# Optimization experiments

Hardware: AMD Instinct MI355X
Metric: run time of the kernel (lower is better)

## Reference

```python
import jax, jax.numpy as jnp
import numpy as np

D_MODEL = 1024


def setup_inputs() -> dict:
    key = jax.random.key(0)
    kx, kq, kk, kv = jax.random.split(key, 4)
    x = jax.random.normal(kx, (4, 2048, D_MODEL), dtype=jnp.float32)
    s = 1.0 / np.sqrt(D_MODEL)
    # torch nn.Linear weight is [out, in]; y = x @ W.T
    Wq = jax.random.normal(kq, (D_MODEL, D_MODEL), dtype=jnp.float32) * s
    Wk = jax.random.normal(kk, (D_MODEL, D_MODEL), dtype=jnp.float32) * s
    Wv = jax.random.normal(kv, (D_MODEL, D_MODEL), dtype=jnp.float32) * s
    return {"x": x, "Wq": Wq, "Wk": Wk, "Wv": Wv}


def reference(x, Wq, Wk, Wv):
    # Linear projections (no bias): [b, s, d]
    Q = jnp.einsum("bsd,ed->bse", x, Wq)
    K = jnp.einsum("bsd,ed->bse", x, Wk)
    V = jnp.einsum("bsd,ed->bse", x, Wv)
    d_k = Q.shape[-1]
    scores = jnp.einsum("bqd,bkd->bqk", Q, K) / jnp.sqrt(jnp.asarray(d_k, Q.dtype))
    weights = jax.nn.softmax(scores, axis=-1)
    return jnp.einsum("bqk,bkd->bqd", weights, V)
```

## Files before the change

### kernel.cpp

```cpp
#include <hip/hip_runtime.h>
#include <hip/hip_bf16.h>

using bf16 = __hip_bfloat16;
typedef __attribute__((ext_vector_type(8))) short short8;
typedef __attribute__((ext_vector_type(16))) float f32x16;

__global__ __launch_bounds__(256) void cast_all(const float* __restrict__ x,
                                                const float* __restrict__ Wq,
                                                const float* __restrict__ Wk,
                                                const float* __restrict__ Wv,
                                                bf16* __restrict__ xb, bf16* __restrict__ Wb) {
  const int b = blockIdx.x;
  const float* src;
  bf16* dst;
  if (b < 8192) {
    src = x + (size_t)b * 1024;
    dst = xb + (size_t)b * 1024;
  } else if (b < 9216) {
    src = Wq + (size_t)(b - 8192) * 1024;
    dst = Wb + (size_t)(b - 8192) * 1024;
  } else if (b < 10240) {
    src = Wk + (size_t)(b - 9216) * 1024;
    dst = Wb + (size_t)(b - 8192) * 1024;
  } else {
    src = Wv + (size_t)(b - 10240) * 1024;
    dst = Wb + (size_t)(b - 8192) * 1024;
  }
  const int i = threadIdx.x * 4;
  const float4 f = *(const float4*)(src + i);
  bf16 h[4];
  h[0] = __float2bfloat16(f.x);
  h[1] = __float2bfloat16(f.y);
  h[2] = __float2bfloat16(f.z);
  h[3] = __float2bfloat16(f.w);
  *(uint2*)(dst + i) = *(const uint2*)h;
}

template <int BN, class Epi>
__device__ __forceinline__ void gemm_nt(const bf16* __restrict__ A, const bf16* __restrict__ B,
                                        int lda, int ldb, int K, int m0, int n0, Epi epi) {
  constexpr int THREADS = BN * 2;
  constexpr int NA = 8192 / (THREADS * 16);
  constexpr int NB = (BN * 64) / (THREADS * 16);
  constexpr int L = NA + NB;
  constexpr int SLOT = (128 + BN) * 64;
  __shared__ char smem[3 * SLOT];
  const int t = threadIdx.x;
  const int lane = t & 63;
  const int wave = t >> 6;
  const int wm = (BN == 256) ? (wave >> 2) * 64 : (wave >> 1) * 64;
  const int wn = (BN == 256) ? (wave & 3) * 64 : (wave & 1) * 64;
  const int rl = lane & 31;
  const int grp = lane >> 5;

  f32x16 acc[2][2];
#pragma unroll
  for (int i = 0; i < 2; ++i)
#pragma unroll
    for (int j = 0; j < 2; ++j)
#pragma unroll
      for (int r = 0; r < 16; ++r) acc[i][j][r] = 0.f;

  const bf16* gA[NA];
#pragma unroll
  for (int j = 0; j < NA; ++j) {
    const int s = j * THREADS + t;
    const int row = s >> 2;
    const int f = (row + (row >> 2)) & 3;
    gA[j] = A + (size_t)(m0 + row) * lda + ((((s & 3) ^ f)) << 3);
  }
  const bf16* gB[NB];
#pragma unroll
  for (int j = 0; j < NB; ++j) {
    const int s = j * THREADS + t;
    const int row = s >> 2;
    const int f = (row + (row >> 2)) & 3;
    gB[j] = B + (size_t)(n0 + row) * ldb + ((((s & 3) ^ f)) << 3);
  }

  auto stage = [&](int kt, int slot) {
    char* base = smem + slot * SLOT;
    bf16* As = (bf16*)base;
    bf16* Bs = (bf16*)(base + 8192);
    const int k0 = kt * 32;
#pragma unroll
    for (int j = 0; j < NA; ++j)
      __builtin_amdgcn_global_load_lds(
          (const __attribute__((address_space(1))) unsigned int*)(gA[j] + k0),
          (__attribute__((address_space(3))) unsigned int*)(As + (j * THREADS + wave * 64) * 8),
          16, 0, 0);
#pragma unroll
    for (int j = 0; j < NB; ++j)
      __builtin_amdgcn_global_load_lds(
          (const __attribute__((address_space(1))) unsigned int*)(gB[j] + k0),
          (__attribute__((address_space(3))) unsigned int*)(Bs + (j * THREADS + wave * 64) * 8),
          16, 0, 0);
  };

  const int NT = K >> 5;

  stage(0, 0);
  stage(1, 1);
  if constexpr (L == 3) {
    asm volatile("s_waitcnt vmcnt(3)" ::: "memory");
  } else {
    asm volatile("s_waitcnt vmcnt(4)" ::: "memory");
  }
  __builtin_amdgcn_s_barrier();
  __builtin_amdgcn_sched_barrier(0);

  int s0 = 0;
  for (int kt = 0; kt < NT; ++kt) {
    const int s1 = (s0 == 2) ? 0 : s0 + 1;
    const int s2 = (s1 == 2) ? 0 : s1 + 1;
    const char* base = smem + s0 * SLOT;
    const bf16* As = (const bf16*)base;
    const bf16* Bs = (const bf16*)(base + 8192);

    if (kt + 2 < NT) stage(kt + 2, s2);

    short8 af[2][2], bv[2][2];
#pragma unroll
    for (int ks = 0; ks < 2; ++ks) {
      const int kb = ks * 2 + grp;
#pragma unroll
      for (int mt = 0; mt < 2; ++mt) {
        const int rowa = wm + mt * 32 + rl;
        const int fa = (rowa + (rowa >> 2)) & 3;
        af[ks][mt] = *(const short8*)(As + rowa * 32 + ((kb ^ fa) << 3));
        const int rowb = wn + mt * 32 + rl;
        const int fb = (rowb + (rowb >> 2)) & 3;
        bv[ks][mt] = *(const short8*)(Bs + rowb * 32 + ((kb ^ fb) << 3));
      }
    }
    __builtin_amdgcn_s_setprio(1);
#pragma unroll
    for (int ks = 0; ks < 2; ++ks)
#pragma unroll
      for (int mt = 0; mt < 2; ++mt)
#pragma unroll
        for (int nt = 0; nt < 2; ++nt)
          acc[mt][nt] = __builtin_amdgcn_mfma_f32_32x32x16_bf16(af[ks][mt], bv[ks][nt],
                                                                acc[mt][nt], 0, 0, 0);
    __builtin_amdgcn_s_setprio(0);
    if (kt + 1 < NT) {
      if (kt + 2 < NT) {
        if constexpr (L == 3) {
          asm volatile("s_waitcnt vmcnt(3) lgkmcnt(0)" ::: "memory");
        } else {
          asm volatile("s_waitcnt vmcnt(4) lgkmcnt(0)" ::: "memory");
        }
      } else {
        asm volatile("s_waitcnt vmcnt(0) lgkmcnt(0)" ::: "memory");
      }
      __builtin_amdgcn_s_barrier();
      __builtin_amdgcn_sched_barrier(0);
    }
    s0 = s1;
  }
  __syncthreads();

  epi(acc, m0, n0, wm, wn, lane, wave, smem);
}

__device__ __forceinline__ int c_row(int reg, int lane) {
  return (reg & 3) + 8 * (reg >> 2) + 4 * (lane >> 5);
}

template <class F>
__device__ __forceinline__ void for_each_c(const f32x16 (&acc)[2][2], int wm, int wn, int lane,
                                           F f) {
  const int rl = lane & 31;
#pragma unroll
  for (int mt = 0; mt < 2; ++mt)
#pragma unroll
    for (int nt = 0; nt < 2; ++nt)
#pragma unroll
      for (int reg = 0; reg < 16; ++reg)
        f(wm + mt * 32 + c_row(reg, lane), wn + nt * 32 + rl, acc[mt][nt][reg]);
}

__global__ __launch_bounds__(512, 4) void proj_kernel(const bf16* __restrict__ xb,
                                                      const bf16* __restrict__ Wb,
                                                      bf16* __restrict__ Qb,
                                                      bf16* __restrict__ Kb,
                                                      bf16* __restrict__ Vt) {
  const int id = blockIdx.y * 12 + blockIdx.x;
  const int g = id & 7, s = id >> 3;
  const int m0 = (g * 8 + (s & 7)) * 128;
  const int n0 = (s >> 3) * 256;
  gemm_nt<256>(xb, Wb, 1024, 1024, 1024, m0, n0,
          [=](const f32x16 (&acc)[2][2], int m0, int n0, int wm, int wn, int lane, int wave,
              char* smem) {
    if (n0 < 2048) {
      bf16* dst = (n0 < 1024) ? Qb : Kb;
      const int nb = (n0 < 1024) ? n0 : (n0 - 1024);
      for_each_c(acc, wm, wn, lane, [&](int m, int n, float v) {
        dst[(size_t)(m0 + m) * 1024 + nb + n] = __float2bfloat16(v);
      });
    } else {
      bf16* T = (bf16*)(smem) + wave * 2304;
      const int rl = lane & 31;
      const int g4 = 4 * (lane >> 5);
      const int mbase = m0 + wm;
      const int bb = mbase >> 11;
      const int sbase = mbase & 2047;
      const int nvbase = n0 - 2048 + wn;
#pragma unroll
      for (int p = 0; p < 2; ++p) {
#pragma unroll
        for (int mt = 0; mt < 2; ++mt)
#pragma unroll
          for (int q = 0; q < 4; ++q) {
            bf16 h4[4];
#pragma unroll
            for (int r = 0; r < 4; ++r) h4[r] = __float2bfloat16(acc[mt][p][4 * q + r]);
            *(uint2*)(T + rl * 72 + mt * 32 + 8 * q + g4) = *(const uint2*)h4;
          }
        asm volatile("s_waitcnt lgkmcnt(0)" ::: "memory");
#pragma unroll
        for (int i = 0; i < 4; ++i) {
          const int nl = i * 8 + (lane >> 3);
          const int ml = (lane & 7) * 8;
          const short8 val = *(const short8*)(T + nl * 72 + ml);
          *(short8*)(Vt + ((size_t)bb * 1024 + nvbase + p * 32 + nl) * 2048 + sbase + ml) = val;
        }
        asm volatile("s_waitcnt lgkmcnt(0)" ::: "memory");
      }
    }
  });
}

__global__ __launch_bounds__(512, 4) void qk_exp_kernel(const bf16* __restrict__ Qb,
                                                        const bf16* __restrict__ Kb,
                                                        bf16* __restrict__ E,
                                                        float* __restrict__ Lpart) {
  const int z = blockIdx.y;
  const int id2 = blockIdx.x;
  const int g = id2 & 7, s = id2 >> 3;
  const int m0 = ((g & 3) * 4 + (s & 3)) * 128;
  const int n0 = ((g >> 2) * 4 + (s >> 2)) * 256;
  const bf16* A = Qb + (size_t)z * 2048 * 1024;
  const bf16* B = Kb + (size_t)z * 2048 * 1024;
  bf16* Ez = E + (size_t)z * 2048 * 2048;
  float* Lz = Lpart + (size_t)z * 8 * 2048;
  gemm_nt<256>(A, B, 1024, 1024, 1024, m0, n0,
          [=](const f32x16 (&acc)[2][2], int m0, int n0, int wm, int wn, int lane, int wave,
              char* smem) {
    float* Lp = (float*)smem;
    const int rl = lane & 31;
#pragma unroll
    for (int mt = 0; mt < 2; ++mt)
#pragma unroll
      for (int reg = 0; reg < 16; ++reg) {
        const int mr = wm + mt * 32 + c_row(reg, lane);
        float s2 = 0.f;
#pragma unroll
        for (int nt = 0; nt < 2; ++nt) {
          const float e = __expf(acc[mt][nt][reg] * 0.03125f);
          Ez[(size_t)(m0 + mr) * 2048 + n0 + wn + nt * 32 + rl] = __float2bfloat16(e);
          s2 += e;
        }
        s2 += __shfl_xor(s2, 1, 64);
        s2 += __shfl_xor(s2, 2, 64);
        s2 += __shfl_xor(s2, 4, 64);
        s2 += __shfl_xor(s2, 8, 64);
        s2 += __shfl_xor(s2, 16, 64);
        if (rl == 0) Lp[mr * 4 + (wave & 3)] = s2;
      }
    __syncthreads();
    const int t = threadIdx.x;
    if (t < 128)
      Lz[(n0 >> 8) * 2048 + m0 + t] =
          Lp[t * 4 + 0] + Lp[t * 4 + 1] + Lp[t * 4 + 2] + Lp[t * 4 + 3];
  });
}

__global__ __launch_bounds__(512, 4) void pv_kernel(const bf16* __restrict__ E,
                                                    const bf16* __restrict__ Vt,
                                                    const float* __restrict__ Lpart,
                                                    float* __restrict__ out) {
  const int z = blockIdx.y;
  const int id2 = blockIdx.x;
  const int g = id2 & 7, s = id2 >> 3;
  const int m0 = ((g & 3) * 4 + (s & 3)) * 128;
  const int n0 = ((g >> 2) * 2 + (s >> 2)) * 256;
  const bf16* A = E + (size_t)z * 2048 * 2048;
  const bf16* B = Vt + (size_t)z * 1024 * 2048;
  const float* Lz = Lpart + (size_t)z * 8 * 2048;
  float* oz = out + (size_t)z * 2048 * 1024;
  gemm_nt<256>(A, B, 2048, 2048, 2048, m0, n0,
          [=](const f32x16 (&acc)[2][2], int m0, int n0, int wm, int wn, int lane, int wave,
              char* smem) {
    float* Lsm = (float*)smem;
    const int t = threadIdx.x;
    if (t < 128) {
      float s2 = 0.f;
#pragma unroll
      for (int i = 0; i < 8; ++i) s2 += Lz[(size_t)i * 2048 + m0 + t];
      Lsm[t] = 1.f / s2;
    }
    __syncthreads();
    const int rl = lane & 31;
#pragma unroll
    for (int mt = 0; mt < 2; ++mt)
#pragma unroll
      for (int reg = 0; reg < 16; ++reg) {
        const int ml = wm + mt * 32 + c_row(reg, lane);
        const float il = Lsm[ml];
#pragma unroll
        for (int nt = 0; nt < 2; ++nt)
          oz[(size_t)(m0 + ml) * 1024 + n0 + wn + nt * 32 + rl] = acc[mt][nt][reg] * il;
      }
  });
}

extern "C" void kernel_launch(void* const* d_in, const int* in_sizes, int n_in,
                              void* d_out, int out_size, void* d_ws, size_t ws_size,
                              hipStream_t stream) {
  const float* x = (const float*)d_in[0];
  const float* Wq = (const float*)d_in[1];
  const float* Wk = (const float*)d_in[2];
  const float* Wv = (const float*)d_in[3];
  float* out = (float*)d_out;

  char* w = (char*)d_ws;
  bf16* xb = (bf16*)w; w += (size_t)8192 * 1024 * 2;
  bf16* Wb = (bf16*)w; w += (size_t)3072 * 1024 * 2;
  bf16* Qb = (bf16*)w; w += (size_t)8192 * 1024 * 2;
  bf16* Kb = (bf16*)w; w += (size_t)8192 * 1024 * 2;
  bf16* Vt = (bf16*)w; w += (size_t)8192 * 1024 * 2;
  bf16* E  = (bf16*)w; w += (size_t)4 * 2048 * 2048 * 2;
  float* Lpart = (float*)w; w += (size_t)4 * 8 * 2048 * 4;

  cast_all<<<11264, 256, 0, stream>>>(x, Wq, Wk, Wv, xb, Wb);

  proj_kernel<<<dim3(12, 64), 512, 0, stream>>>(xb, Wb, Qb, Kb, Vt);

  qk_exp_kernel<<<dim3(128, 4), 512, 0, stream>>>(Qb, Kb, E, Lpart);

  pv_kernel<<<dim3(64, 4), 512, 0, stream>>>(E, Vt, Lpart, out);
}
```

Measured before the change: 229.2 us.

## Use 256x256 GEMM tiles for projection and QK kernels

Adds a gemm256 routine that computes a 256x256 output tile per 512-thread block, with each wave holding a 128x64 accumulator (4x2 MFMA 32x32 tiles). The projection and QK-exp kernels switch to it, cutting their grids in half and raising arithmetic intensity so each loaded A/B tile is reused across twice as many outputs. The trade-off is more accumulator registers (launch bounds drop to 2 blocks per CU), 96KB of LDS per block, and fewer blocks in the grid, which may leave CUs underfilled on the 256-block QK launch.

```diff
diff --git a/kernel.cpp b/kernel.cpp
--- a/kernel.cpp
+++ b/kernel.cpp
@@ -36,6 +36,119 @@
   *(uint2*)(dst + i) = *(const uint2*)h;
 }
 
+template <class Epi>
+__device__ __forceinline__ void gemm256(const bf16* __restrict__ A, const bf16* __restrict__ B,
+                                        int lda, int ldb, int K, int m0, int n0, Epi epi) {
+  constexpr int SLOT = 32768;
+  __shared__ char smem[3 * SLOT];
+  const int t = threadIdx.x;
+  const int lane = t & 63;
+  const int wave = t >> 6;
+  const int wr = wave >> 2;
+  const int wc = wave & 3;
+  const int rl = lane & 31;
+  const int grp = lane >> 5;
+
+  f32x16 acc[4][2];
+#pragma unroll
+  for (int i = 0; i < 4; ++i)
+#pragma unroll
+    for (int j = 0; j < 2; ++j)
+#pragma unroll
+      for (int r = 0; r < 16; ++r) acc[i][j][r] = 0.f;
+
+  const bf16* gA[2];
+  const bf16* gB[2];
+#pragma unroll
+  for (int j = 0; j < 2; ++j) {
+    const int s = j * 512 + t;
+    const int row = s >> 2;
+    const int f = (row + (row >> 2)) & 3;
+    const int c = ((s & 3) ^ f) << 3;
+    gA[j] = A + (size_t)(m0 + row) * lda + c;
+    gB[j] = B + (size_t)(n0 + row) * ldb + c;
+  }
+
+  auto stage = [&](int kt, int slot) {
+    char* base = smem + slot * SLOT;
+    bf16* As = (bf16*)base;
+    bf16* Bs = (bf16*)(base + 16384);
+    const int k0 = kt * 32;
+#pragma unroll
+    for (int j = 0; j < 2; ++j)
+      __builtin_amdgcn_global_load_lds(
+          (const __attribute__((address_space(1))) unsigned int*)(gA[j] + k0),
+          (__attribute__((address_space(3))) unsigned int*)(As + (j * 512 + wave * 64) * 8),
+          16, 0, 0);
+#pragma unroll
+    for (int j = 0; j < 2; ++j)
+      __builtin_amdgcn_global_load_lds(
+          (const __attribute__((address_space(1))) unsigned int*)(gB[j] + k0),
+          (__attribute__((address_space(3))) unsigned int*)(Bs + (j * 512 + wave * 64) * 8),
+          16, 0, 0);
+  };
+
+  const int NT = K >> 5;
+
+  stage(0, 0);
+  stage(1, 1);
+  asm volatile("s_waitcnt vmcnt(4)" ::: "memory");
+  __builtin_amdgcn_s_barrier();
+  __builtin_amdgcn_sched_barrier(0);
+
+  int s0 = 0;
+  for (int kt = 0; kt < NT; ++kt) {
+    const int s1 = (s0 == 2) ? 0 : s0 + 1;
+    const int s2 = (s1 == 2) ? 0 : s1 + 1;
+    const char* base = smem + s0 * SLOT;
+    const bf16* As = (const bf16*)base;
+    const bf16* Bs = (const bf16*)(base + 16384);
+
+    if (kt + 2 < NT) stage(kt + 2, s2);
+
+    short8 af[2][4], bv[2][2];
+#pragma unroll
+    for (int ks = 0; ks < 2; ++ks) {
+      const int kb = ks * 2 + grp;
+#pragma unroll
+      for (int mt = 0; mt < 4; ++mt) {
+        const int rowa = wr * 128 + mt * 32 + rl;
+        const int fa = (rowa + (rowa >> 2)) & 3;
+        af[ks][mt] = *(const short8*)(As + rowa * 32 + ((kb ^ fa) << 3));
+      }
+#pragma unroll
+      for (int nt = 0; nt < 2; ++nt) {
+        const int rowb = wc * 64 + nt * 32 + rl;
+        const int fb = (rowb + (rowb >> 2)) & 3;
+        bv[ks][nt] = *(const short8*)(Bs + rowb * 32 + ((kb ^ fb) << 3));
+      }
+    }
+    __builtin_amdgcn_s_setprio(1);
+#pragma unroll
+    for (int ks = 0; ks < 2; ++ks)
+#pragma unroll
+      for (int mt = 0; mt < 4; ++mt)
+#pragma unroll
+        for (int nt = 0; nt < 2; ++nt)
+          acc[mt][nt] = __builtin_amdgcn_mfma_f32_32x32x16_bf16(af[ks][mt], bv[ks][nt],
+                                                                acc[mt][nt], 0, 0, 0);
+    __builtin_amdgcn_s_setprio(0);
+    if (kt + 1 < NT) {
+      if (kt + 2 < NT) {
+        asm volatile("s_waitcnt vmcnt(4) lgkmcnt(0)" ::: "memory");
+      } else {
+        asm volatile("s_waitcnt vmcnt(0) lgkmcnt(0)" ::: "memory");
+      }
+      __builtin_amdgcn_s_barrier();
+      __builtin_amdgcn_sched_barrier(0);
+    }
+    s0 = s1;
+  }
+  __syncthreads();
+
+  epi(acc, m0, n0, wr, wc, lane, wave, (char*)smem);
+}
+
 template <int BN, class Epi>
 __device__ __forceinline__ void gemm_nt(const bf16* __restrict__ A, const bf16* __restrict__ B,
                                         int lda, int ldb, int K, int m0, int n0, Epi epi) {
@@ -48,8 +161,8 @@
   const int t = threadIdx.x;
   const int lane = t & 63;
   const int wave = t >> 6;
-  const int wm = (BN == 256) ? (wave >> 2) * 64 : (wave >> 1) * 64;
-  const int wn = (BN == 256) ? (wave & 3) * 64 : (wave & 1) * 64;
+  const int wm = (wave >> 2) * 64;
+  const int wn = (wave & 3) * 64;
   const int rl = lane & 31;
   const int grp = lane >> 5;
 
@@ -168,8 +281,8 @@
 }
 
 template <class F>
-__device__ __forceinline__ void for_each_c(const f32x16 (&acc)[2][2], int wm, int wn, int lane,
-                                           F f) {
+__device__ __forceinline__ void for_each_c2(const f32x16 (&acc)[2][2], int wm, int wn, int lane,
+                                            F f) {
   const int rl = lane & 31;
 #pragma unroll
   for (int mt = 0; mt < 2; ++mt)
@@ -180,85 +293,96 @@
         f(wm + mt * 32 + c_row(reg, lane), wn + nt * 32 + rl, acc[mt][nt][reg]);
 }
 
-__global__ __launch_bounds__(512, 4) void proj_kernel(const bf16* __restrict__ xb,
+__global__ __launch_bounds__(512, 2) void proj_kernel(const bf16* __restrict__ xb,
                                                       const bf16* __restrict__ Wb,
                                                       bf16* __restrict__ Qb,
                                                       bf16* __restrict__ Kb,
                                                       bf16* __restrict__ Vt) {
-  const int id = blockIdx.y * 12 + blockIdx.x;
+  const int id = blockIdx.x;
   const int g = id & 7, s = id >> 3;
-  const int m0 = (g * 8 + (s & 7)) * 128;
-  const int n0 = (s >> 3) * 256;
-  gemm_nt<256>(xb, Wb, 1024, 1024, 1024, m0, n0,
-          [=](const f32x16 (&acc)[2][2], int m0, int n0, int wm, int wn, int lane, int wave,
+  const int m0 = (g * 4 + (s & 3)) * 256;
+  const int n0 = (s >> 2) * 256;
+  gemm256(xb, Wb, 1024, 1024, 1024, m0, n0,
+          [=](const f32x16 (&acc)[4][2], int m0, int n0, int wr, int wc, int lane, int wave,
               char* smem) {
+    const int rl = lane & 31;
     if (n0 < 2048) {
       bf16* dst = (n0 < 1024) ? Qb : Kb;
-      const int nb = (n0 < 1024) ? n0 : (n0 - 1024);
-      for_each_c(acc, wm, wn, lane, [&](int m, int n, float v) {
-        dst[(size_t)(m0 + m) * 1024 + nb + n] = __float2bfloat16(v);
-      });
+      const int nb = n0 & 1023;
+#pragma unroll
+      for (int mt = 0; mt < 4; ++mt)
+#pragma unroll
+        for (int nt = 0; nt < 2; ++nt)
+#pragma unroll
+          for (int reg = 0; reg < 16; ++reg) {
+            const int m = wr * 128 + mt * 32 + c_row(reg, lane);
+            const int n = wc * 64 + nt * 32 + rl;
+            dst[(size_t)(m0 + m) * 1024 + nb + n] = __float2bfloat16(acc[mt][nt][reg]);
+          }
     } else {
-      bf16* T = (bf16*)(smem) + wave * 2304;
-      const int rl = lane & 31;
+      bf16* T = (bf16*)smem + wave * 2304;
       const int g4 = 4 * (lane >> 5);
-      const int mbase = m0 + wm;
-      const int bb = mbase >> 11;
-      const int sbase = mbase & 2047;
-      const int nvbase = n0 - 2048 + wn;
-#pragma unroll
-      for (int p = 0; p < 2; ++p) {
-#pragma unroll
-        for (int mt = 0; mt < 2; ++mt)
-#pragma unroll
-          for (int q = 0; q < 4; ++q) {
-            bf16 h4[4];
-#pragma unroll
-            for (int r = 0; r < 4; ++r) h4[r] = __float2bfloat16(acc[mt][p][4 * q + r]);
-            *(uint2*)(T + rl * 72 + mt * 32 + 8 * q + g4) = *(const uint2*)h4;
+      const int nvbase = n0 - 2048 + wc * 64;
+#pragma unroll
+      for (int h = 0; h < 2; ++h) {
+        const int mbase = m0 + wr * 128 + h * 64;
+        const int bb = mbase >> 11;
+        const int sbase = mbase & 2047;
+#pragma unroll
+        for (int p = 0; p < 2; ++p) {
+#pragma unroll
+          for (int mt = 0; mt < 2; ++mt)
+#pragma unroll
+            for (int q = 0; q < 4; ++q) {
+              bf16 h4[4];
+#pragma unroll
+              for (int r = 0; r < 4; ++r)
+                h4[r] = __float2bfloat16(acc[h * 2 + mt][p][4 * q + r]);
+              *(uint2*)(T + rl * 72 + mt * 32 + 8 * q + g4) = *(const uint2*)h4;
+            }
+          asm volatile("s_waitcnt lgkmcnt(0)" ::: "memory");
+#pragma unroll
+          for (int i = 0; i < 4; ++i) {
+            const int nl = i * 8 + (lane >> 3);
+            const int ml = (lane & 7) * 8;
+            const short8 val = *(const short8*)(T + nl * 72 + ml);
+            *(short8*)(Vt + ((size_t)bb * 1024 + nvbase + p * 32 + nl) * 2048 + sbase + ml) = val;
           }
-        asm volatile("s_waitcnt lgkmcnt(0)" ::: "memory");
-#pragma unroll
-        for (int i = 0; i < 4; ++i) {
-          const int nl = i * 8 + (lane >> 3);
-          const int ml = (lane & 7) * 8;
-          const short8 val = *(const short8*)(T + nl * 72 + ml);
-          *(short8*)(Vt + ((size_t)bb * 1024 + nvbase + p * 32 + nl) * 2048 + sbase + ml) = val;
+          asm volatile("s_waitcnt lgkmcnt(0)" ::: "memory");
         }
-        asm volatile("s_waitcnt lgkmcnt(0)" ::: "memory");
       }
     }
   });
 }
 
-__global__ __launch_bounds__(512, 4) void qk_exp_kernel(const bf16* __restrict__ Qb,
+__global__ __launch_bounds__(512, 2) void qk_exp_kernel(const bf16* __restrict__ Qb,
                                                         const bf16* __restrict__ Kb,
                                                         bf16* __restrict__ E,
                                                         float* __restrict__ Lpart) {
   const int z = blockIdx.y;
   const int id2 = blockIdx.x;
   const int g = id2 & 7, s = id2 >> 3;
-  const int m0 = ((g & 3) * 4 + (s & 3)) * 128;
-  const int n0 = ((g >> 2) * 4 + (s >> 2)) * 256;
+  const int m0 = ((g & 3) * 2 + (s & 1)) * 256;
+  const int n0 = ((g >> 2) * 4 + (s >> 1)) * 256;
   const bf16* A = Qb + (size_t)z * 2048 * 1024;
   const bf16* B = Kb + (size_t)z * 2048 * 1024;
   bf16* Ez = E + (size_t)z * 2048 * 2048;
   float* Lz = Lpart + (size_t)z * 8 * 2048;
-  gemm_nt<256>(A, B, 1024, 1024, 1024, m0, n0,
-          [=](const f32x16 (&acc)[2][2], int m0, int n0, int wm, int wn, int lane, int wave,
+  gemm256(A, B, 1024, 1024, 1024, m0, n0,
+          [=](const f32x16 (&acc)[4][2], int m0, int n0, int wr, int wc, int lane, int wave,
               char* smem) {
     float* Lp = (float*)smem;
     const int rl = lane & 31;
 #pragma unroll
-    for (int mt = 0; mt < 2; ++mt)
+    for (int mt = 0; mt < 4; ++mt)
 #pragma unroll
       for (int reg = 0; reg < 16; ++reg) {
-        const int mr = wm + mt * 32 + c_row(reg, lane);
+        const int mr = wr * 128 + mt * 32 + c_row(reg, lane);
         float s2 = 0.f;
 #pragma unroll
         for (int nt = 0; nt < 2; ++nt) {
           const float e = __expf(acc[mt][nt][reg] * 0.03125f);
-          Ez[(size_t)(m0 + mr) * 2048 + n0 + wn + nt * 32 + rl] = __float2bfloat16(e);
+          Ez[(size_t)(m0 + mr) * 2048 + n0 + wc * 64 + nt * 32 + rl] = __float2bfloat16(e);
           s2 += e;
         }
         s2 += __shfl_xor(s2, 1, 64);
@@ -266,11 +390,11 @@
         s2 += __shfl_xor(s2, 4, 64);
         s2 += __shfl_xor(s2, 8, 64);
         s2 += __shfl_xor(s2, 16, 64);
-        if (rl == 0) Lp[mr * 4 + (wave & 3)] = s2;
+        if (rl == 0) Lp[mr * 4 + wc] = s2;
       }
     __syncthreads();
     const int t = threadIdx.x;
-    if (t < 128)
+    if (t < 256)
       Lz[(n0 >> 8) * 2048 + m0 + t] =
           Lp[t * 4 + 0] + Lp[t * 4 + 1] + Lp[t * 4 + 2] + Lp[t * 4 + 3];
   });
@@ -335,9 +459,9 @@
 
   cast_all<<<11264, 256, 0, stream>>>(x, Wq, Wk, Wv, xb, Wb);
 
-  proj_kernel<<<dim3(12, 64), 512, 0, stream>>>(xb, Wb, Qb, Kb, Vt);
-
-  qk_exp_kernel<<<dim3(128, 4), 512, 0, stream>>>(Qb, Kb, E, Lpart);
+  proj_kernel<<<384, 512, 0, stream>>>(xb, Wb, Qb, Kb, Vt);
+
+  qk_exp_kernel<<<dim3(64, 4), 512, 0, stream>>>(Qb, Kb, E, Lpart);
 
   pv_kernel<<<dim3(64, 4), 512, 0, stream>>>(E, Vt, Lpart, out);
 }
```

Measured after the change: 240.4 us. +4.9%, slower.
